# Performance work log

Hardware: AMD Instinct MI355X
Metric: run time of the kernel (lower is better)

Reference implementation:

```python
import jax, jax.numpy as jnp
import numpy as np

EPS = 1e-12

def _spectral_normalize(W, u):
    # torch spectral_norm (eval-time math): v = normalize(W^T u), sigma = u^T W v
    u = jax.lax.stop_gradient(u)
    v = W.T @ u
    v = jax.lax.stop_gradient(v / (jnp.linalg.norm(v) + EPS))
    sigma = u @ (W @ v)
    return W / sigma

def _conv1x1(x, W):
    # 1x1 conv, no bias: (out,in) x (B,in,H,W) -> (B,out,H,W)
    return jnp.einsum('oc,bchw->bohw', W, x)

def setup_inputs() -> dict:
    key = jax.random.key(0)
    ks = jax.random.split(key, 10)
    B, C, H, W = 4, 512, 64, 64
    Cp = C // 8
    return {
        'x': jax.random.normal(ks[0], (B, C, H, W), jnp.float32),
        'Wf': jax.random.normal(ks[1], (Cp, C), jnp.float32) * 0.05,
        'Wg': jax.random.normal(ks[2], (Cp, C), jnp.float32) * 0.05,
        'Wh': jax.random.normal(ks[3], (Cp, C), jnp.float32) * 0.05,
        'Wv': jax.random.normal(ks[4], (C, Cp), jnp.float32) * 0.05,
        'uf': jax.random.normal(ks[5], (Cp,), jnp.float32),
        'ug': jax.random.normal(ks[6], (Cp,), jnp.float32),
        'uh': jax.random.normal(ks[7], (Cp,), jnp.float32),
        'uv': jax.random.normal(ks[8], (C,), jnp.float32),
        'gamma': jax.random.normal(ks[9], (1,), jnp.float32) * 0.1,
    }

def reference(x, Wf, Wg, Wh, Wv, uf, ug, uh, uv, gamma):
    B, C, H, W = x.shape
    Cp = Wf.shape[0]
    N = H * W
    Wf_sn = _spectral_normalize(Wf, uf)
    Wg_sn = _spectral_normalize(Wg, ug)
    Wh_sn = _spectral_normalize(Wh, uh)
    Wv_sn = _spectral_normalize(Wv, uv)
    fx = _conv1x1(x, Wf_sn).reshape(B, Cp, N)   # (B,Cp,N)
    gx = _conv1x1(x, Wg_sn).reshape(B, Cp, N)   # (B,Cp,N)
    # fx^T gx: (B,N,N), unscaled single-head attention, softmax over last dim
    scores = jnp.einsum('bcn,bcm->bnm', fx, gx)
    attn = jax.nn.softmax(scores, axis=-1)
    hx = _conv1x1(x, Wh_sn).reshape(B, Cp, N)
    # hx @ attn: out[b,c,j] = sum_i hx[b,c,i] * attn[b,i,j]
    out = jnp.einsum('bci,bij->bcj', hx, attn).reshape(B, Cp, H, W)
    unscaled = _conv1x1(out, Wv_sn)
    return gamma * unscaled + x
```

## Files before the change

### kernel.cpp

```cpp
#include <hip/hip_runtime.h>


#define NB 4
#define CC 512
#define CP 64
#define NN 4096
#define L2E 1.4426950408889634f

typedef __attribute__((ext_vector_type(8))) short short8;
typedef __attribute__((ext_vector_type(4))) float floatx4;
typedef __attribute__((ext_vector_type(16))) float floatx16;

#define MFMA32(A, B, C) __builtin_amdgcn_mfma_f32_32x32x16_bf16((A), (B), (C), 0, 0, 0)

__device__ __forceinline__ float bf2f_u(unsigned short h) {
    return __uint_as_float((unsigned)h << 16);
}
__device__ __forceinline__ float bf16lo(unsigned v) { return __uint_as_float(v << 16); }
__device__ __forceinline__ float bf16hi(unsigned v) { return __uint_as_float(v & 0xffff0000u); }
__device__ __forceinline__ unsigned short f2bf(float f) {
    unsigned u = __float_as_uint(f);
    u += 0x7fffu + ((u >> 16) & 1u);
    return (unsigned short)(u >> 16);
}
__device__ __forceinline__ unsigned pack2bf(float a, float b) {
    return (unsigned)f2bf(a) | ((unsigned)f2bf(b) << 16);
}
__device__ __forceinline__ float ldS(const void* p, long i, int f32) {
    return f32 ? ((const float*)p)[i] : bf2f_u(((const unsigned short*)p)[i]);
}
__device__ __forceinline__ float4 ld4(const void* p, long i, int f32) {
    if (f32) return *reinterpret_cast<const float4*>((const float*)p + i);
    uint2 v = *reinterpret_cast<const uint2*>((const unsigned short*)p + i);
    return make_float4(bf16lo(v.x), bf16hi(v.x), bf16lo(v.y), bf16hi(v.y));
}
__device__ __forceinline__ short8 frag8(const void* p, long i, int f32) {
    uint4 au;
    if (f32) {
        float4 v0 = *reinterpret_cast<const float4*>((const float*)p + i);
        float4 v1 = *reinterpret_cast<const float4*>((const float*)p + i + 4);
        au.x = pack2bf(v0.x, v0.y); au.y = pack2bf(v0.z, v0.w);
        au.z = pack2bf(v1.x, v1.y); au.w = pack2bf(v1.z, v1.w);
    } else {
        au = *reinterpret_cast<const uint4*>((const unsigned short*)p + i);
    }
    return *reinterpret_cast<short8*>(&au);
}
__device__ __forceinline__ short8 as_s8(uint4 v) { return *reinterpret_cast<short8*>(&v); }
__device__ __forceinline__ floatx16 zero16() {
    floatx16 z;
    #pragma unroll
    for (int i = 0; i < 16; ++i) z[i] = 0.f;
    return z;
}
__device__ __forceinline__ unsigned cvtpk_bf16(float a, float b) {
    unsigned r;
    asm("v_cvt_pk_bf16_f32 %0, %1, %2" : "=v"(r) : "v"(a), "v"(b));
    return r;
}
__device__ __forceinline__ void pl32swap(unsigned &a, unsigned &b) {
    asm("v_permlane32_swap_b32 %0, %1" : "+v"(a), "+v"(b));
}
__device__ __forceinline__ float rcpf(float x) {
    float r;
    asm("v_rcp_f32 %0, %1" : "=v"(r) : "v"(x));
    return r;
}
__device__ __forceinline__ float exp2a(float x) {
    float r;
    asm("v_exp_f32 %0, %1" : "=v"(r) : "v"(x));
    return r;
}

__global__ __launch_bounds__(256) void detect_kernel(
    const unsigned* __restrict__ x, int* __restrict__ flag)
{
    __shared__ int red[256];
    const int t = threadIdx.x;
    int bad = 0;
    for (int i = t; i < 4096; i += 256) {
        unsigned w = x[i];
        float f0 = __uint_as_float(w << 16);
        float f1 = __uint_as_float(w & 0xffff0000u);
        float a0 = fabsf(f0), a1 = fabsf(f1);
        if (!(a0 <= 1e3f) || (f0 != 0.f && a0 < 1e-20f)) bad++;
        if (!(a1 <= 1e3f) || (f1 != 0.f && a1 < 1e-20f)) bad++;
    }
    red[t] = bad;
    __syncthreads();
    for (int s = 128; s > 0; s >>= 1) { if (t < s) red[t] += red[t + s]; __syncthreads(); }
    if (t == 0) *flag = (red[0] > 64) ? 1 : 0;
}

__global__ __launch_bounds__(256) void xpose_kernel(
    const void* __restrict__ x, const int* __restrict__ dflag,
    unsigned short* __restrict__ xTF)
{
    const int f32 = *dflag;
    const int nt = blockIdx.x;
    const int b  = blockIdx.y;
    const int n0 = nt * 32;
    const int t = threadIdx.x;
    __shared__ unsigned short xl[32][72];

    const int n_l = t & 31, cg8 = ((t >> 5) & 7) * 8;
    const int q = t >> 6, lo = t & 63;

    for (int slab = 0; slab < 8; ++slab) {
        const int cs = slab * 64;
        float v[8];
        #pragma unroll
        for (int j = 0; j < 8; ++j)
            v[j] = ldS(x, ((long)b * CC + cs + cg8 + j) * NN + n0 + n_l, f32);
        if (slab) __syncthreads();
        unsigned* row = reinterpret_cast<unsigned*>(&xl[n_l][cg8]);
        row[0] = pack2bf(v[0], v[1]);
        row[1] = pack2bf(v[2], v[3]);
        row[2] = pack2bf(v[4], v[5]);
        row[3] = pack2bf(v[6], v[7]);
        __syncthreads();
        const int cb = q * 16 + ((lo >> 5) << 3);
        uint4 val = *reinterpret_cast<const uint4*>(&xl[lo & 31][cb]);
        size_t off = (((size_t)(b * 128 + nt) * 32) + slab * 4 + q) * 512 + (size_t)lo * 8;
        *reinterpret_cast<uint4*>(xTF + off) = val;
    }
}

__global__ __launch_bounds__(512) void sigma_kernel(
    const void* __restrict__ Wf, const void* __restrict__ Wg,
    const void* __restrict__ Wh, const void* __restrict__ Wv,
    const void* __restrict__ uf, const void* __restrict__ ug,
    const void* __restrict__ uh, const void* __restrict__ uv,
    const int* __restrict__ dflag, float* __restrict__ sig)
{
    const int f32 = *dflag;
    const int w = blockIdx.x;
    const void* W;
    const void* u;
    if (w == 0)      { W = Wf; u = uf; }
    else if (w == 1) { W = Wg; u = ug; }
    else if (w == 2) { W = Wh; u = uh; }
    else             { W = Wv; u = uv; }

    __shared__ float us[512];
    __shared__ float red[512];
    const int t = threadIdx.x;
    float S;

    if (w < 3) {
        if (t < 64) us[t] = ldS(u, t, f32);
        __syncthreads();
        float a = 0.f;
        #pragma unroll
        for (int i = 0; i < 64; ++i)
            a = fmaf(ldS(W, (long)i * 512 + t, f32), us[i], a);
        red[t] = a * a;
        __syncthreads();
        #pragma unroll
        for (int s = 256; s > 0; s >>= 1) {
            if (t < s) red[t] += red[t + s];
            __syncthreads();
        }
        S = red[0];
    } else {
        us[t] = ldS(u, t, f32);
        __syncthreads();
        const int g = t >> 6, c = t & 63;
        float a = 0.f;
        #pragma unroll
        for (int k = 0; k < 64; ++k) {
            int i = g + k * 8;
            a = fmaf(ldS(W, (long)i * 64 + c, f32), us[i], a);
        }
        red[t] = a;
        __syncthreads();
        #pragma unroll
        for (int s = 256; s >= 64; s >>= 1) {
            if (t < s) red[t] += red[t + s];
            __syncthreads();
        }
        float ac = (t < 64) ? red[t] : 0.f;
        __syncthreads();
        red[t] = ac * ac;
        __syncthreads();
        #pragma unroll
        for (int s = 256; s > 0; s >>= 1) {
            if (t < s) red[t] += red[t + s];
            __syncthreads();
        }
        S = red[0];
    }
    if (t == 0) sig[w] = (sqrtf(S) + 1e-12f) / S;
}

__global__ __launch_bounds__(256) void wprep_kernel(
    const void* __restrict__ Wf, const void* __restrict__ Wg,
    const void* __restrict__ Wh,
    const int* __restrict__ dflag, const float* __restrict__ sig,
    unsigned short* __restrict__ WF)
{
    const int f32 = *dflag;
    const int idx = blockIdx.x * 256 + threadIdx.x;
    const int l   = idx & 63;
    const int kc  = (idx >> 6) & 31;
    const int cpt = (idx >> 11) & 1;
    const int wi  = idx >> 12;
    const void* W = (wi == 0) ? Wf : ((wi == 1) ? Wg : Wh);
    const float sc = sig[wi] * (wi == 0 ? L2E : 1.f);
    const int cp = cpt * 32 + (l & 31);
    const int c  = kc * 16 + ((l >> 5) << 3);
    const long base = (long)cp * CC + c;
    float a0 = ldS(W, base + 0, f32) * sc, a1 = ldS(W, base + 1, f32) * sc;
    float a2 = ldS(W, base + 2, f32) * sc, a3 = ldS(W, base + 3, f32) * sc;
    float a4 = ldS(W, base + 4, f32) * sc, a5 = ldS(W, base + 5, f32) * sc;
    float a6 = ldS(W, base + 6, f32) * sc, a7 = ldS(W, base + 7, f32) * sc;
    uint4 o;
    o.x = pack2bf(a0, a1); o.y = pack2bf(a2, a3);
    o.z = pack2bf(a4, a5); o.w = pack2bf(a6, a7);
    *reinterpret_cast<uint4*>(WF + (size_t)idx * 8) = o;
}

__global__ __launch_bounds__(256, 4) void proj_kernel(
    const unsigned short* __restrict__ xTF,
    const unsigned short* __restrict__ WF,
    unsigned short* __restrict__ fxF, unsigned short* __restrict__ gxF,
    unsigned short* __restrict__ hxF)
{
    const int t = threadIdx.x;
    const int w = t >> 6, l = t & 63;
    const int b  = blockIdx.y;
    const int zc = blockIdx.z;
    const int wi = zc >> 1, cpt = zc & 1;
    const int nt = blockIdx.x * 4 + w;

    const unsigned short* xb = xTF + ((size_t)(b * 128 + nt) * 32) * 512 + (size_t)l * 8;
    const unsigned short* wb = WF + ((size_t)zc * 32) * 512 + (size_t)l * 8;

    floatx16 accE = zero16(), accO = zero16();
    uint4 x0 = *reinterpret_cast<const uint4*>(xb);
    uint4 w0 = *reinterpret_cast<const uint4*>(wb);
    uint4 x1, w1;

    if (wi == 2) {
        for (int kc = 0; kc < 32; kc += 2) {
            x1 = *reinterpret_cast<const uint4*>(xb + (kc + 1) * 512);
            w1 = *reinterpret_cast<const uint4*>(wb + (kc + 1) * 512);
            accE = MFMA32(as_s8(x0), as_s8(w0), accE);
            if (kc + 2 < 32) {
                x0 = *reinterpret_cast<const uint4*>(xb + (kc + 2) * 512);
                w0 = *reinterpret_cast<const uint4*>(wb + (kc + 2) * 512);
            }
            accO = MFMA32(as_s8(x1), as_s8(w1), accO);
        }
    } else {
        for (int kc = 0; kc < 32; kc += 2) {
            x1 = *reinterpret_cast<const uint4*>(xb + (kc + 1) * 512);
            w1 = *reinterpret_cast<const uint4*>(wb + (kc + 1) * 512);
            accE = MFMA32(as_s8(w0), as_s8(x0), accE);
            if (kc + 2 < 32) {
                x0 = *reinterpret_cast<const uint4*>(xb + (kc + 2) * 512);
                w0 = *reinterpret_cast<const uint4*>(wb + (kc + 2) * 512);
            }
            accO = MFMA32(as_s8(w1), as_s8(x1), accO);
        }
    }

    float a[16];
    #pragma unroll
    for (int i = 0; i < 16; ++i) a[i] = accE[i] + accO[i];

    if (wi < 2) {
        unsigned short* __restrict__ dstF = (wi == 0) ? fxF : gxF;
        #pragma unroll
        for (int kcl = 0; kcl < 2; ++kcl) {
            const int r8 = kcl * 8;
            unsigned u0 = cvtpk_bf16(a[r8 + 0], a[r8 + 1]);
            unsigned u1 = cvtpk_bf16(a[r8 + 2], a[r8 + 3]);
            unsigned u2 = cvtpk_bf16(a[r8 + 4], a[r8 + 5]);
            unsigned u3 = cvtpk_bf16(a[r8 + 6], a[r8 + 7]);
            pl32swap(u0, u2);
            pl32swap(u1, u3);
            uint4 o = make_uint4(u0, u1, u2, u3);
            size_t off = (((size_t)(b * 128 + nt) * 4) + cpt * 2 + kcl) * 512 + (size_t)l * 8;
            *reinterpret_cast<uint4*>(dstF + off) = o;
        }
    } else {
        #pragma unroll
        for (int ich = 0; ich < 2; ++ich) {
            const int r8 = ich * 8;
            unsigned u0 = cvtpk_bf16(a[r8 + 0], a[r8 + 1]);
            unsigned u1 = cvtpk_bf16(a[r8 + 2], a[r8 + 3]);
            unsigned u2 = cvtpk_bf16(a[r8 + 4], a[r8 + 5]);
            unsigned u3 = cvtpk_bf16(a[r8 + 6], a[r8 + 7]);
            pl32swap(u0, u2);
            pl32swap(u1, u3);
            uint4 o = make_uint4(u0, u1, u2, u3);
            size_t off = ((((size_t)(b * 128 + nt) * 2 + ich) * 2) + cpt) * 512 + (size_t)l * 8;
            *reinterpret_cast<uint4*>(hxF + off) = o;
        }
    }
}

__global__ __launch_bounds__(256, 4) void rowstats_kernel(
    const unsigned short* __restrict__ fxF, const unsigned short* __restrict__ gxF,
    float* __restrict__ rl)
{
    const int t = threadIdx.x;
    const int w = t >> 6, l = t & 63, l31 = l & 31, hi = l >> 5;
    const int b = blockIdx.z;
    const int i0 = blockIdx.x * 128 + w * 32;
    const int jbase = blockIdx.y * (NN / 8);

    const unsigned short* fA = fxF + ((size_t)(b * 128 + (i0 >> 5))) * 2048 + (size_t)l * 8;
    uint4 af[4];
    #pragma unroll
    for (int kc = 0; kc < 4; ++kc)
        af[kc] = *reinterpret_cast<const uint4*>(fA + kc * 512);

    const unsigned short* gB = gxF + ((size_t)(b * 128 + (jbase >> 5))) * 2048 + (size_t)l * 8;

    float suml[16];
    #pragma unroll
    for (int r = 0; r < 16; ++r) suml[r] = 0.f;

    uint4 bf0[4], bf1[4];
    auto loadB = [&](uint4* bf, int jt) {
        const unsigned short* p = gB + (size_t)jt * 2048;
        #pragma unroll
        for (int kc = 0; kc < 4; ++kc)
            bf[kc] = *reinterpret_cast<const uint4*>(p + kc * 512);
    };
    auto bodyR = [&](uint4* bf) {
        floatx16 s = zero16();
        #pragma unroll
        for (int kc = 0; kc < 4; ++kc)
            s = MFMA32(as_s8(af[kc]), as_s8(bf[kc]), s);
        #pragma unroll
        for (int r = 0; r < 16; ++r) suml[r] += exp2a(s[r]);
    };

    loadB(bf0, 0);
    for (int jt = 0; jt < 16; jt += 2) {
        loadB(bf1, jt + 1);
        bodyR(bf0);
        if (jt + 2 < 16) loadB(bf0, jt + 2);
        bodyR(bf1);
    }

    #pragma unroll
    for (int r = 0; r < 16; ++r) {
        float v = suml[r];
        v += __shfl_xor(v, 1);
        v += __shfl_xor(v, 2);
        v += __shfl_xor(v, 4);
        v += __shfl_xor(v, 8);
        v += __shfl_xor(v, 16);
        suml[r] = v;
    }
    if (l31 == 0) {
        #pragma unroll
        for (int r = 0; r < 16; ++r) {
            int row = (r & 3) + 8 * (r >> 2) + 4 * hi;
            atomicAdd(&rl[(size_t)b * NN + i0 + row], suml[r]);
        }
    }
}

__global__ __launch_bounds__(256) void scalehx_kernel(
    const float* __restrict__ rl, unsigned short* __restrict__ hxF)
{
    const int idx = blockIdx.x * 256 + threadIdx.x;
    const int l = idx & 63;
    const int r = idx >> 6;
    const int ich = (r >> 1) & 1;
    const int tile = (r >> 2) & 127;
    const int b = r >> 9;
    const int i0 = tile * 32 + ich * 16 + (l >> 5) * 8;
    const float* rp = rl + (size_t)b * NN + i0;
    float4 ra = *reinterpret_cast<const float4*>(rp);
    float4 rb = *reinterpret_cast<const float4*>(rp + 4);
    uint4 v = *reinterpret_cast<uint4*>(hxF + (size_t)idx * 8);
    uint4 ov;
    ov.x = pack2bf(bf16lo(v.x) * rcpf(ra.x), bf16hi(v.x) * rcpf(ra.y));
    ov.y = pack2bf(bf16lo(v.y) * rcpf(ra.z), bf16hi(v.y) * rcpf(ra.w));
    ov.z = pack2bf(bf16lo(v.z) * rcpf(rb.x), bf16hi(v.z) * rcpf(rb.y));
    ov.w = pack2bf(bf16lo(v.w) * rcpf(rb.z), bf16hi(v.w) * rcpf(rb.w));
    *reinterpret_cast<uint4*>(hxF + (size_t)idx * 8) = ov;
}

__global__ __launch_bounds__(256, 4) void pv_kernel(
    const unsigned short* __restrict__ fxF, const unsigned short* __restrict__ gxF,
    const unsigned short* __restrict__ hxF,
    float* __restrict__ opF0, float* __restrict__ opF1,
    float* __restrict__ opF2, float* __restrict__ opF3)
{
    const int t = threadIdx.x;
    const int w = t >> 6, l = t & 63, l31 = l & 31, hi = l >> 5;
    const int igrp = w >> 1, jgrp = w & 1;
    const int b = blockIdx.z;
    const int j0 = blockIdx.x * 64;
    const int isb = blockIdx.y;
    const int tbase = isb * 32 + igrp * 16;

    __shared__ float red[64 * 64];

    uint4 qf[4];
    {
        const unsigned short* gq =
            gxF + ((size_t)(b * 128 + (j0 >> 5) + jgrp)) * 2048 + (size_t)l * 8;
        #pragma unroll
        for (int kc = 0; kc < 4; ++kc)
            qf[kc] = *reinterpret_cast<const uint4*>(gq + kc * 512);
    }

    floatx16 acc0 = zero16(), acc1 = zero16();

    const unsigned short* fb = fxF + ((size_t)(b * 128 + tbase)) * 2048 + (size_t)l * 8;
    const unsigned short* vb = hxF + ((size_t)(b * 128 + tbase)) * 2048 + (size_t)l * 8;

    #pragma unroll 2
    for (int it = 0; it < 16; ++it) {
        const unsigned short* fp = fb + (size_t)it * 2048;
        const unsigned short* vp = vb + (size_t)it * 2048;
        uint4 af[4], vf[4];
        #pragma unroll
        for (int kc = 0; kc < 4; ++kc)
            af[kc] = *reinterpret_cast<const uint4*>(fp + kc * 512);
        vf[0] = *reinterpret_cast<const uint4*>(vp);
        vf[1] = *reinterpret_cast<const uint4*>(vp + 1024);
        vf[2] = *reinterpret_cast<const uint4*>(vp + 512);
        vf[3] = *reinterpret_cast<const uint4*>(vp + 1536);

        floatx16 s = zero16();
        #pragma unroll
        for (int kc = 0; kc < 4; ++kc)
            s = MFMA32(as_s8(af[kc]), as_s8(qf[kc]), s);

        float e[16];
        #pragma unroll
        for (int r = 0; r < 16; ++r) e[r] = exp2a(s[r]);

        unsigned u0 = cvtpk_bf16(e[0], e[1]);
        unsigned u1 = cvtpk_bf16(e[2], e[3]);
        unsigned u2 = cvtpk_bf16(e[4], e[5]);
        unsigned u3 = cvtpk_bf16(e[6], e[7]);
        pl32swap(u0, u2);
        pl32swap(u1, u3);
        uint4 pa0 = make_uint4(u0, u1, u2, u3);
        unsigned u4 = cvtpk_bf16(e[8], e[9]);
        unsigned u5 = cvtpk_bf16(e[10], e[11]);
        unsigned u6 = cvtpk_bf16(e[12], e[13]);
        unsigned u7 = cvtpk_bf16(e[14], e[15]);
        pl32swap(u4, u6);
        pl32swap(u5, u7);
        uint4 pa1 = make_uint4(u4, u5, u6, u7);

        acc0 = MFMA32(as_s8(pa0), as_s8(vf[0]), acc0);
        acc0 = MFMA32(as_s8(pa1), as_s8(vf[1]), acc0);
        acc1 = MFMA32(as_s8(pa0), as_s8(vf[2]), acc1);
        acc1 = MFMA32(as_s8(pa1), as_s8(vf[3]), acc1);
    }

    #pragma unroll
    for (int q = 0; q < 4; ++q)
        *reinterpret_cast<float4*>(&red[(q * 256 + t) * 4]) =
            make_float4(0.f, 0.f, 0.f, 0.f);
    __syncthreads();
    #pragma unroll
    for (int r = 0; r < 16; ++r) {
        int row = jgrp * 32 + (r & 3) + 8 * (r >> 2) + 4 * hi;
        atomicAdd(&red[row * 64 + l31],      acc0[r]);
        atomicAdd(&red[row * 64 + 32 + l31], acc1[r]);
    }
    __syncthreads();

    float* __restrict__ dst = (isb == 0) ? opF0 : ((isb == 1) ? opF1 : ((isb == 2) ? opF2 : opF3));
    #pragma unroll
    for (int q = 0; q < 4; ++q) {
        int idx = q * 256 + t;
        int e2  = idx & 1;
        int ll  = (idx >> 1) & 63;
        int ks  = (idx >> 7) & 1;
        int ntl = idx >> 8;
        int jloc = ntl * 16 + (ll & 15);
        int cp   = ks * 32 + ((ll >> 4) << 3) + e2 * 4;
        float4 v = *reinterpret_cast<const float4*>(&red[jloc * 64 + cp]);
        size_t off = (((size_t)(b * 256 + (j0 >> 4) + ntl) * 2 + ks) * 64 + ll) * 8 + e2 * 4;
        *reinterpret_cast<float4*>(dst + off) = v;
    }
}

__global__ __launch_bounds__(256) void outproj_kernel(
    const void* __restrict__ x,
    const void* __restrict__ Wv,
    const void* __restrict__ gamma,
    const int* __restrict__ dflag,
    const float* __restrict__ sig,
    const float* __restrict__ opF0, const float* __restrict__ opF1,
    const float* __restrict__ opF2, const float* __restrict__ opF3,
    void* __restrict__ y)
{
    const int f32 = *dflag;
    const int n0     = blockIdx.x * 64;
    const int cobase = blockIdx.y * 128;
    const int b      = blockIdx.z;
    const int t = threadIdx.x;
    const int wv = t >> 6, l = t & 63, l15 = l & 15, quad = l >> 4;
    const float scale = ldS(gamma, 0, f32) * sig[3];

    floatx4 acc[4][2];
    #pragma unroll
    for (int ns = 0; ns < 4; ++ns)
        #pragma unroll
        for (int ct = 0; ct < 2; ++ct) acc[ns][ct] = (floatx4){0.f, 0.f, 0.f, 0.f};

    #pragma unroll
    for (int ks = 0; ks < 2; ++ks) {
        short8 a[4];
        #pragma unroll
        for (int ns = 0; ns < 4; ++ns) {
            size_t fo = (((size_t)(b * 256 + (n0 >> 4) + ns) * 2 + ks) * 64 + l) * 8;
            float4 s0 = *reinterpret_cast<const float4*>(opF0 + fo);
            float4 s1 = *reinterpret_cast<const float4*>(opF1 + fo);
            float4 s2 = *reinterpret_cast<const float4*>(opF2 + fo);
            float4 s3 = *reinterpret_cast<const float4*>(opF3 + fo);
            float4 t0 = *reinterpret_cast<const float4*>(opF0 + fo + 4);
            float4 t1 = *reinterpret_cast<const float4*>(opF1 + fo + 4);
            float4 t2 = *reinterpret_cast<const float4*>(opF2 + fo + 4);
            float4 t3 = *reinterpret_cast<const float4*>(opF3 + fo + 4);
            float v0 = s0.x + s1.x + s2.x + s3.x;
            float v1 = s0.y + s1.y + s2.y + s3.y;
            float v2 = s0.z + s1.z + s2.z + s3.z;
            float v3 = s0.w + s1.w + s2.w + s3.w;
            float v4 = t0.x + t1.x + t2.x + t3.x;
            float v5 = t0.y + t1.y + t2.y + t3.y;
            float v6 = t0.z + t1.z + t2.z + t3.z;
            float v7 = t0.w + t1.w + t2.w + t3.w;
            uint4 au;
            au.x = pack2bf(v0, v1); au.y = pack2bf(v2, v3);
            au.z = pack2bf(v4, v5); au.w = pack2bf(v6, v7);
            a[ns] = *reinterpret_cast<short8*>(&au);
        }
        const int kb = ks * 32 + quad * 8;
        #pragma unroll
        for (int ct = 0; ct < 2; ++ct) {
            const int co = cobase + 32 * wv + 16 * ct + l15;
            short8 bfr = frag8(Wv, (long)co * CP + kb, f32);
            #pragma unroll
            for (int ns = 0; ns < 4; ++ns)
                acc[ns][ct] = __builtin_amdgcn_mfma_f32_16x16x32_bf16(
                    a[ns], bfr, acc[ns][ct], 0, 0, 0);
        }
    }

    #pragma unroll
    for (int ns = 0; ns < 4; ++ns)
        #pragma unroll
        for (int ct = 0; ct < 2; ++ct) {
            const int co = cobase + 32 * wv + 16 * ct + l15;
            const long base = ((long)b * CC + co) * NN + n0 + 16 * ns + quad * 4;
            float4 xv = ld4(x, base, f32);
            float o0 = fmaf(scale, acc[ns][ct][0], xv.x);
            float o1 = fmaf(scale, acc[ns][ct][1], xv.y);
            float o2 = fmaf(scale, acc[ns][ct][2], xv.z);
            float o3 = fmaf(scale, acc[ns][ct][3], xv.w);
            if (f32) {
                *reinterpret_cast<float4*>((float*)y + base) = make_float4(o0, o1, o2, o3);
            } else {
                uint2 o;
                o.x = pack2bf(o0, o1);
                o.y = pack2bf(o2, o3);
                *reinterpret_cast<uint2*>((unsigned short*)y + base) = o;
            }
        }
}

extern "C" void kernel_launch(void* const* d_in, const int* in_sizes, int n_in,
                              void* d_out, int out_size, void* d_ws, size_t ws_size,
                              hipStream_t stream)
{
    const void* x  = d_in[0];
    const void* Wf = d_in[1];
    const void* Wg = d_in[2];
    const void* Wh = d_in[3];
    const void* Wv = d_in[4];
    const void* uf = d_in[5];
    const void* ug = d_in[6];
    const void* uh = d_in[7];
    const void* uv = d_in[8];
    const void* gm = d_in[9];

    char* base = (char*)d_ws;
    int*   dfl = (int*)(base);
    float* sig = (float*)(base + 512);
    float* rl  = (float*)(base + 1024);
    float* opF0 = (float*)(base + 1024 + 65536);
    float* opF1 = opF0 + (size_t)NB * NN * CP;
    float* opF2 = opF1 + (size_t)NB * NN * CP;
    float* opF3 = opF2 + (size_t)NB * NN * CP;
    unsigned short* fxF = (unsigned short*)(opF3 + (size_t)NB * NN * CP);
    unsigned short* gxF = fxF + (size_t)NB * CP * NN;
    unsigned short* hxF = gxF + (size_t)NB * CP * NN;
    unsigned short* xTF = hxF + (size_t)NB * CP * NN;
    unsigned short* WF  = xTF + (size_t)NB * CC * NN;

    hipMemsetAsync(rl, 0, (size_t)NB * NN * sizeof(float), stream);

    hipLaunchKernelGGL(detect_kernel, dim3(1), dim3(256), 0, stream,
                       (const unsigned*)x, dfl);
    hipLaunchKernelGGL(xpose_kernel, dim3(128, NB), dim3(256), 0, stream,
                       x, dfl, xTF);
    hipLaunchKernelGGL(sigma_kernel, dim3(4), dim3(512), 0, stream,
                       Wf, Wg, Wh, Wv, uf, ug, uh, uv, dfl, sig);
    hipLaunchKernelGGL(wprep_kernel, dim3(48), dim3(256), 0, stream,
                       Wf, Wg, Wh, dfl, sig, WF);
    hipLaunchKernelGGL(proj_kernel, dim3(32, NB, 6), dim3(256), 0, stream,
                       xTF, WF, fxF, gxF, hxF);
    hipLaunchKernelGGL(rowstats_kernel, dim3(NN / 128, 8, NB), dim3(256), 0, stream,
                       fxF, gxF, rl);
    hipLaunchKernelGGL(scalehx_kernel, dim3((NB * CP * NN / 8) / 256), dim3(256), 0, stream,
                       rl, hxF);
    hipLaunchKernelGGL(pv_kernel, dim3(NN / 64, 4, NB), dim3(256), 0, stream,
                       fxF, gxF, hxF, opF0, opF1, opF2, opF3);
    hipLaunchKernelGGL(outproj_kernel, dim3(NN / 64, CC / 128, NB), dim3(256), 0, stream,
                       x, Wv, gm, dfl, sig, opF0, opF1, opF2, opF3, d_out);
}
```

Before: 226.2 us.

## Stage shared K/V tiles in double-buffered LDS in rowstats and pv kernels

In rowstats, all four waves previously loaded the same gx tile from global memory separately. Now each wave loads one quarter and stages it in a double-buffered shared-memory tile read by all waves. In pv, the two waves of each pair split the f and h tile loads and share them through LDS. This cuts redundant global/L2 traffic at the cost of LDS traffic and a block-wide barrier every iteration, which can stall the MFMA pipeline.

```diff
diff --git a/kernel.cpp b/kernel.cpp
--- a/kernel.cpp
+++ b/kernel.cpp
@@ -311,40 +311,46 @@
     const int i0 = blockIdx.x * 128 + w * 32;
     const int jbase = blockIdx.y * (NN / 8);
 
+    __shared__ unsigned short stg[2][2048];
+
     const unsigned short* fA = fxF + ((size_t)(b * 128 + (i0 >> 5))) * 2048 + (size_t)l * 8;
     uint4 af[4];
     #pragma unroll
     for (int kc = 0; kc < 4; ++kc)
         af[kc] = *reinterpret_cast<const uint4*>(fA + kc * 512);
 
-    const unsigned short* gB = gxF + ((size_t)(b * 128 + (jbase >> 5))) * 2048 + (size_t)l * 8;
+    const unsigned short* gB = gxF + ((size_t)(b * 128 + (jbase >> 5))) * 2048
+                               + (size_t)w * 512 + (size_t)l * 8;
 
     float suml[16];
     #pragma unroll
     for (int r = 0; r < 16; ++r) suml[r] = 0.f;
 
-    uint4 bf0[4], bf1[4];
-    auto loadB = [&](uint4* bf, int jt) {
-        const unsigned short* p = gB + (size_t)jt * 2048;
+    uint4 rg = *reinterpret_cast<const uint4*>(gB);
+    *reinterpret_cast<uint4*>(&stg[0][w * 512 + l * 8]) = rg;
+    __syncthreads();
+
+    #pragma unroll 2
+    for (int jt = 0; jt < 16; ++jt) {
+        const int cur = jt & 1;
+        if (jt + 1 < 16)
+            rg = *reinterpret_cast<const uint4*>(gB + (size_t)(jt + 1) * 2048);
+
+        uint4 bf[4];
         #pragma unroll
         for (int kc = 0; kc < 4; ++kc)
-            bf[kc] = *reinterpret_cast<const uint4*>(p + kc * 512);
-    };
-    auto bodyR = [&](uint4* bf) {
+            bf[kc] = *reinterpret_cast<const uint4*>(&stg[cur][kc * 512 + l * 8]);
+
         floatx16 s = zero16();
         #pragma unroll
         for (int kc = 0; kc < 4; ++kc)
             s = MFMA32(as_s8(af[kc]), as_s8(bf[kc]), s);
         #pragma unroll
         for (int r = 0; r < 16; ++r) suml[r] += exp2a(s[r]);
-    };
-
-    loadB(bf0, 0);
-    for (int jt = 0; jt < 16; jt += 2) {
-        loadB(bf1, jt + 1);
-        bodyR(bf0);
-        if (jt + 2 < 16) loadB(bf0, jt + 2);
-        bodyR(bf1);
+
+        if (jt + 1 < 16)
+            *reinterpret_cast<uint4*>(&stg[cur ^ 1][w * 512 + l * 8]) = rg;
+        __syncthreads();
     }
 
     #pragma unroll
@@ -402,7 +408,8 @@
     const int isb = blockIdx.y;
     const int tbase = isb * 32 + igrp * 16;
 
-    __shared__ float red[64 * 64];
+    __shared__ unsigned short stg[2][2][2][2048];
+    float* red = reinterpret_cast<float*>(stg);
 
     uint4 qf[4];
     {
@@ -415,21 +422,43 @@
 
     floatx16 acc0 = zero16(), acc1 = zero16();
 
-    const unsigned short* fb = fxF + ((size_t)(b * 128 + tbase)) * 2048 + (size_t)l * 8;
-    const unsigned short* vb = hxF + ((size_t)(b * 128 + tbase)) * 2048 + (size_t)l * 8;
+    const unsigned short* sb =
+        (jgrp == 0 ? fxF : hxF) + ((size_t)(b * 128 + tbase)) * 2048 + (size_t)l * 8;
+
+    uint4 rg0 = *reinterpret_cast<const uint4*>(sb);
+    uint4 rg1 = *reinterpret_cast<const uint4*>(sb + 512);
+    uint4 rg2 = *reinterpret_cast<const uint4*>(sb + 1024);
+    uint4 rg3 = *reinterpret_cast<const uint4*>(sb + 1536);
+    {
+        unsigned short* d = &stg[igrp][0][jgrp][l * 8];
+        *reinterpret_cast<uint4*>(d)        = rg0;
+        *reinterpret_cast<uint4*>(d + 512)  = rg1;
+        *reinterpret_cast<uint4*>(d + 1024) = rg2;
+        *reinterpret_cast<uint4*>(d + 1536) = rg3;
+    }
+    __syncthreads();
 
     #pragma unroll 2
     for (int it = 0; it < 16; ++it) {
-        const unsigned short* fp = fb + (size_t)it * 2048;
-        const unsigned short* vp = vb + (size_t)it * 2048;
+        const int cur = it & 1;
+        if (it + 1 < 16) {
+            const unsigned short* p = sb + (size_t)(it + 1) * 2048;
+            rg0 = *reinterpret_cast<const uint4*>(p);
+            rg1 = *reinterpret_cast<const uint4*>(p + 512);
+            rg2 = *reinterpret_cast<const uint4*>(p + 1024);
+            rg3 = *reinterpret_cast<const uint4*>(p + 1536);
+        }
+
+        const unsigned short* fl = &stg[igrp][cur][0][l * 8];
+        const unsigned short* vl = &stg[igrp][cur][1][l * 8];
         uint4 af[4], vf[4];
         #pragma unroll
         for (int kc = 0; kc < 4; ++kc)
-            af[kc] = *reinterpret_cast<const uint4*>(fp + kc * 512);
-        vf[0] = *reinterpret_cast<const uint4*>(vp);
-        vf[1] = *reinterpret_cast<const uint4*>(vp + 1024);
-        vf[2] = *reinterpret_cast<const uint4*>(vp + 512);
-        vf[3] = *reinterpret_cast<const uint4*>(vp + 1536);
+            af[kc] = *reinterpret_cast<const uint4*>(fl + kc * 512);
+        vf[0] = *reinterpret_cast<const uint4*>(vl);
+        vf[1] = *reinterpret_cast<const uint4*>(vl + 1024);
+        vf[2] = *reinterpret_cast<const uint4*>(vl + 512);
+        vf[3] = *reinterpret_cast<const uint4*>(vl + 1536);
 
         floatx16 s = zero16();
         #pragma unroll
@@ -459,6 +488,15 @@
         acc0 = MFMA32(as_s8(pa1), as_s8(vf[1]), acc0);
         acc1 = MFMA32(as_s8(pa0), as_s8(vf[2]), acc1);
         acc1 = MFMA32(as_s8(pa1), as_s8(vf[3]), acc1);
+
+        if (it + 1 < 16) {
+            unsigned short* d = &stg[igrp][cur ^ 1][jgrp][l * 8];
+            *reinterpret_cast<uint4*>(d)        = rg0;
+            *reinterpret_cast<uint4*>(d + 512)  = rg1;
+            *reinterpret_cast<uint4*>(d + 1024) = rg2;
+            *reinterpret_cast<uint4*>(d + 1536) = rg3;
+        }
+        __syncthreads();
     }
 
     #pragma unroll
```

New measurement: 226.4 us. No clear change (+0.1%).
